# Optimization experiments

Hardware: AMD Instinct MI355X
Metric: run time of the kernel (lower is better)

The kernel has to match this reference:

```python
import jax, jax.numpy as jnp
import numpy as np

B, T, W, D, NT = 32, 512, 250, 768, 2  # batch, subtokens, words, sim_dim, num_tags


def setup_inputs() -> dict:
    key = jax.random.key(0)
    ks = jax.random.split(key, 20)
    s = 0.05
    # words_ids: 2 subtokens per word for W words, rest padding (-100)
    pos = jnp.arange(T)
    wid = jnp.where(pos < 2 * W, pos // 2, -100).astype(jnp.int64)
    words_ids = jnp.broadcast_to(wid, (B, T))
    inp = {
        'bert_out': jax.random.normal(ks[0], (B, T, D), jnp.float32),
        'words_ids': words_ids,
        'label_detect': jax.random.randint(ks[1], (B, W), 0, NT).astype(jnp.int64),
        'w_ih_l0': jax.random.normal(ks[2], (4 * D, D), jnp.float32) * s,
        'w_hh_l0': jax.random.normal(ks[3], (4 * D, D), jnp.float32) * s,
        'b_l0': jax.random.normal(ks[4], (4 * D,), jnp.float32) * s,
        'w_ih_l0r': jax.random.normal(ks[5], (4 * D, D), jnp.float32) * s,
        'w_hh_l0r': jax.random.normal(ks[6], (4 * D, D), jnp.float32) * s,
        'b_l0r': jax.random.normal(ks[7], (4 * D,), jnp.float32) * s,
        'w_ih_l1': jax.random.normal(ks[8], (4 * D, 2 * D), jnp.float32) * s,
        'w_hh_l1': jax.random.normal(ks[9], (4 * D, D), jnp.float32) * s,
        'b_l1': jax.random.normal(ks[10], (4 * D,), jnp.float32) * s,
        'w_ih_l1r': jax.random.normal(ks[11], (4 * D, 2 * D), jnp.float32) * s,
        'w_hh_l1r': jax.random.normal(ks[12], (4 * D, D), jnp.float32) * s,
        'b_l1r': jax.random.normal(ks[13], (4 * D,), jnp.float32) * s,
        'w_lin': jax.random.normal(ks[14], (NT, 2 * D), jnp.float32) * s,
        'b_lin': jax.random.normal(ks[15], (NT,), jnp.float32) * s,
        'crf_start': jax.random.normal(ks[16], (NT,), jnp.float32) * 0.1,
        'crf_end': jax.random.normal(ks[17], (NT,), jnp.float32) * 0.1,
        'crf_trans': jax.random.normal(ks[18], (NT, NT), jnp.float32) * 0.1,
    }
    return inp


def first_subtoken_gather(bert_out, words_ids):
    # For each word w in [0, W): embedding of its FIRST subtoken.
    # (matches torch.unique(sorted)+first-element-per-group on HF word_ids)
    pos = jnp.arange(T)
    mask = words_ids[:, None, :] == jnp.arange(W)[None, :, None]  # [B, W, T]
    first_idx = jnp.min(jnp.where(mask, pos[None, None, :], T - 1), axis=-1)  # [B, W]
    return jnp.take_along_axis(bert_out, first_idx[..., None], axis=1)  # [B, W, D]


def lstm_dir(x, w_ih, w_hh, b, reverse):
    # x: [B, S, In] -> [B, S, H]; PyTorch gate order i, f, g, o
    H = w_hh.shape[1]
    pre = jnp.einsum('bsi,gi->bsg', x, w_ih) + b  # b = b_ih + b_hh
    if reverse:
        pre = pre[:, ::-1]
    def step(carry, p_t):
        h, c = carry
        g = p_t + h @ w_hh.T
        i, f, gg, o = jnp.split(g, 4, axis=-1)
        c = jax.nn.sigmoid(f) * c + jax.nn.sigmoid(i) * jnp.tanh(gg)
        h = jax.nn.sigmoid(o) * jnp.tanh(c)
        return (h, c), h
    h0 = jnp.zeros((x.shape[0], H), x.dtype)
    _, hs = jax.lax.scan(step, (h0, h0), jnp.swapaxes(pre, 0, 1))
    hs = jnp.swapaxes(hs, 0, 1)
    if reverse:
        hs = hs[:, ::-1]
    return hs


def crf_log_likelihood(emis, tags, start, end, trans):
    # emis: [B, S, K]; tags: [B, S]; mask = all ones; reduction='mean'
    S = emis.shape[1]
    # numerator
    t0 = tags[:, 0]
    emis_score = jnp.sum(jnp.take_along_axis(emis, tags[..., None], axis=-1)[..., 0], axis=1)
    trans_score = jnp.sum(trans[tags[:, :-1], tags[:, 1:]], axis=1)
    num = start[t0] + emis_score + trans_score + end[tags[:, -1]]
    # partition (forward algorithm)
    alpha0 = start[None, :] + emis[:, 0]  # [B, K]
    def step(alpha, e_t):
        alpha = jax.nn.logsumexp(alpha[:, :, None] + trans[None] + e_t[:, None, :], axis=1)
        return alpha, None
    alpha, _ = jax.lax.scan(step, alpha0, jnp.swapaxes(emis[:, 1:], 0, 1))
    logZ = jax.nn.logsumexp(alpha + end[None, :], axis=-1)
    return jnp.mean(num - logZ)


def crf_decode(emis, start, end, trans):
    # Viterbi, mask = all ones. Returns [B, S] int32.
    score0 = start[None, :] + emis[:, 0]
    def fwd(score, e_t):
        cand = score[:, :, None] + trans[None]          # [B, K, K]
        bp = jnp.argmax(cand, axis=1)                    # [B, K]
        score = jnp.max(cand, axis=1) + e_t
        return score, bp
    score, hist = jax.lax.scan(fwd, score0, jnp.swapaxes(emis[:, 1:], 0, 1))
    last = jnp.argmax(score + end[None, :], axis=-1)     # [B]
    def back(tag, bp_t):
        prev = jnp.take_along_axis(bp_t, tag[:, None], axis=1)[:, 0]
        return prev, prev
    _, prevs = jax.lax.scan(back, last, hist, reverse=True)
    path = jnp.concatenate([jnp.swapaxes(prevs, 0, 1), last[:, None]], axis=1)
    return path.astype(jnp.int32)


def reference(bert_out, words_ids, label_detect,
              w_ih_l0, w_hh_l0, b_l0, w_ih_l0r, w_hh_l0r, b_l0r,
              w_ih_l1, w_hh_l1, b_l1, w_ih_l1r, w_hh_l1r, b_l1r,
              w_lin, b_lin, crf_start, crf_end, crf_trans):
    feat = first_subtoken_gather(bert_out, words_ids)                      # [B, W, D]
    h1 = jnp.concatenate([lstm_dir(feat, w_ih_l0, w_hh_l0, b_l0, False),
                          lstm_dir(feat, w_ih_l0r, w_hh_l0r, b_l0r, True)], axis=-1)
    h2 = jnp.concatenate([lstm_dir(h1, w_ih_l1, w_hh_l1, b_l1, False),
                          lstm_dir(h1, w_ih_l1r, w_hh_l1r, b_l1r, True)], axis=-1)
    logits = h2 @ w_lin.T + b_lin                                           # [B, W, 2]
    ner_prob = jax.nn.softmax(logits, axis=-1)
    llh = crf_log_likelihood(ner_prob, label_detect, crf_start, crf_end, crf_trans)
    path = crf_decode(ner_prob, crf_start, crf_end, crf_trans)
    loss = -1.0 * llh
    return path, ner_prob, loss
```

## Files before the change

### kernel.cpp

```cpp
#include <hip/hip_runtime.h>
#include <cmath>

#define B_ 32
#define T_ 512
#define W_ 250
#define D_ 768
#define H_ 768
#define G_ 3072
#define NT_ 2

__global__ void first_idx_kernel(const int* __restrict__ words_ids, int* __restrict__ fidx) {
  int i = blockIdx.x * blockDim.x + threadIdx.x;
  if (i >= B_ * W_) return;
  int b = i / W_, w = i % W_;
  const int* row = words_ids + (size_t)b * T_;
  int idx = T_ - 1;
  for (int t = 0; t < T_; ++t) {
    if (row[t] == w) { idx = t; break; }
  }
  fidx[i] = idx;
}

__global__ void gather_kernel(const float* __restrict__ bert_out, const int* __restrict__ fidx,
                              float* __restrict__ feat) {
  int i = blockIdx.x * blockDim.x + threadIdx.x;
  const int nv = D_ / 4;
  if (i >= B_ * W_ * nv) return;
  int bw = i / nv, d4 = i % nv;
  int b = bw / W_, w = bw % W_;
  int t = fidx[bw];
  float4 v = ((const float4*)(bert_out + ((size_t)b * T_ + t) * D_))[d4];
  ((float4*)(feat + ((size_t)w * B_ + b) * D_))[d4] = v;
}

__global__ __launch_bounds__(256) void gemm_bias_kernel(
    const float* __restrict__ A, const float* __restrict__ Bm,
    const float* __restrict__ bias, float* __restrict__ C,
    int M, int N, int K) {
  __shared__ float As[2][16][132];
  __shared__ float Bs[2][16][132];
  const int tid = threadIdx.x;
  const int row0 = blockIdx.x * 128;
  const int col0 = blockIdx.y * 128;
  const int tx = tid & 15;
  const int ty = tid >> 4;
  const int lr = tid >> 1;
  const int lk = (tid & 1) * 8;

  int ar = row0 + lr;
  if (ar >= M) ar = M - 1;
  const float* __restrict__ Ap = A + (size_t)ar * K + lk;
  const float* __restrict__ Bp = Bm + (size_t)(col0 + lr) * K + lk;

  float acc[8][8];
#pragma unroll
  for (int i = 0; i < 8; ++i)
#pragma unroll
    for (int j = 0; j < 8; ++j) acc[i][j] = 0.0f;

  const int nk = K >> 4;

  {
    float4 a0 = *(const float4*)(Ap + 0);
    float4 a1 = *(const float4*)(Ap + 4);
    float4 b0 = *(const float4*)(Bp + 0);
    float4 b1 = *(const float4*)(Bp + 4);
    As[0][lk + 0][lr] = a0.x; As[0][lk + 1][lr] = a0.y; As[0][lk + 2][lr] = a0.z; As[0][lk + 3][lr] = a0.w;
    As[0][lk + 4][lr] = a1.x; As[0][lk + 5][lr] = a1.y; As[0][lk + 6][lr] = a1.z; As[0][lk + 7][lr] = a1.w;
    Bs[0][lk + 0][lr] = b0.x; Bs[0][lk + 1][lr] = b0.y; Bs[0][lk + 2][lr] = b0.z; Bs[0][lk + 3][lr] = b0.w;
    Bs[0][lk + 4][lr] = b1.x; Bs[0][lk + 5][lr] = b1.y; Bs[0][lk + 6][lr] = b1.z; Bs[0][lk + 7][lr] = b1.w;
  }
  __syncthreads();

  for (int t = 0; t < nk; ++t) {
    const int cur = t & 1;
    float4 a0, a1, b0, b1;
    const bool pf = (t + 1 < nk);
    if (pf) {
      const int k0 = (t + 1) << 4;
      a0 = *(const float4*)(Ap + k0);
      a1 = *(const float4*)(Ap + k0 + 4);
      b0 = *(const float4*)(Bp + k0);
      b1 = *(const float4*)(Bp + k0 + 4);
    }
#pragma unroll
    for (int k = 0; k < 16; ++k) {
      float a[8], b[8];
      *(float4*)&a[0] = *(const float4*)&As[cur][k][ty * 8];
      *(float4*)&a[4] = *(const float4*)&As[cur][k][ty * 8 + 4];
      *(float4*)&b[0] = *(const float4*)&Bs[cur][k][tx * 8];
      *(float4*)&b[4] = *(const float4*)&Bs[cur][k][tx * 8 + 4];
#pragma unroll
      for (int i = 0; i < 8; ++i)
#pragma unroll
        for (int j = 0; j < 8; ++j) acc[i][j] += a[i] * b[j];
    }
    if (pf) {
      const int nxt = cur ^ 1;
      As[nxt][lk + 0][lr] = a0.x; As[nxt][lk + 1][lr] = a0.y; As[nxt][lk + 2][lr] = a0.z; As[nxt][lk + 3][lr] = a0.w;
      As[nxt][lk + 4][lr] = a1.x; As[nxt][lk + 5][lr] = a1.y; As[nxt][lk + 6][lr] = a1.z; As[nxt][lk + 7][lr] = a1.w;
      Bs[nxt][lk + 0][lr] = b0.x; Bs[nxt][lk + 1][lr] = b0.y; Bs[nxt][lk + 2][lr] = b0.z; Bs[nxt][lk + 3][lr] = b0.w;
      Bs[nxt][lk + 4][lr] = b1.x; Bs[nxt][lk + 5][lr] = b1.y; Bs[nxt][lk + 6][lr] = b1.z; Bs[nxt][lk + 7][lr] = b1.w;
    }
    __syncthreads();
  }

#pragma unroll
  for (int i = 0; i < 8; ++i) {
    int r = row0 + ty * 8 + i;
    if (r < M) {
#pragma unroll
      for (int j = 0; j < 8; ++j) {
        int c = col0 + tx * 8 + j;
        C[(size_t)r * N + c] = acc[i][j] + bias[c];
      }
    }
  }
}

__global__ __launch_bounds__(256) void lstm_step_kernel(
    const float* __restrict__ pre_f, const float* __restrict__ pre_r,
    const float* __restrict__ whh_f, const float* __restrict__ whh_r,
    float* __restrict__ out, float* __restrict__ hbuf, float* __restrict__ cbuf,
    int s0, int sl, int Cc) {
  const int wg = blockIdx.x;
  const int dir = wg >> 7;
  const int lw = wg & 127;
  const float* __restrict__ pre = dir ? pre_r : pre_f;
  const float* __restrict__ whh = dir ? whh_r : whh_f;
  float* hb = hbuf + (size_t)dir * 2 * B_ * H_;
  float* cb = cbuf + (size_t)dir * B_ * H_;
  const int tid = threadIdx.x;
  const int u0 = lw * 6;

  const int s = s0 + sl;
  const int w = dir ? (W_ - 1 - s) : s;
  const int prow = dir ? (Cc - 1 - sl) : sl;

  const int rgrp = tid >> 6;
  const int lane = tid & 63;
  const int kgrp = lane >> 3;
  const int bgrp = lane & 7;

  __shared__ float w_lds[24 * 860];
  __shared__ float h_lds[32 * 284];
  __shared__ float g_lds[32][24];

  const int cui = tid >> 5;
  const int cb_ = tid & 31;
  float pre_g0 = 0.f, pre_g1 = 0.f, pre_g2 = 0.f, pre_g3 = 0.f, cprev = 0.f;
  if (tid < 192) {
    const float* pbt = pre + ((size_t)prow * B_ + cb_) * G_;
    pre_g0 = pbt[0 * H_ + u0 + cui];
    pre_g1 = pbt[1 * H_ + u0 + cui];
    pre_g2 = pbt[2 * H_ + u0 + cui];
    pre_g3 = pbt[3 * H_ + u0 + cui];
    if (s > 0) cprev = cb[(size_t)cb_ * H_ + u0 + cui];
  }

  float acc[6][4];
#pragma unroll
  for (int r = 0; r < 6; ++r)
#pragma unroll
    for (int j = 0; j < 4; ++j) acc[r][j] = 0.0f;

  if (s > 0) {
#pragma unroll
    for (int v = 0; v < 18; ++v) {
      int i = v * 256 + tid;
      int r24 = i / 192;
      int f4 = i - r24 * 192;
      int k = f4 * 4;
      int grow = (r24 / 6) * H_ + u0 + (r24 % 6);
      *(float4*)&w_lds[r24 * 860 + k + 4 * (k >> 5)] =
          *(const float4*)(whh + (size_t)grow * H_ + k);
    }

    const float* __restrict__ hprev = hb + (size_t)(s & 1) * B_ * H_;
    const int kl0 = kgrp * 32;

    for (int kc = 0; kc < H_; kc += 256) {
      __syncthreads();
#pragma unroll
      for (int v = 0; v < 8; ++v) {
        int e = v * 1024 + tid * 4;
        int bb = e >> 8;
        int kk = e & 255;
        *(float4*)&h_lds[bb * 284 + kk + 4 * (kk >> 5)] =
            *(const float4*)(hprev + (size_t)bb * H_ + kc + kk);
      }
      __syncthreads();

      const int wbase = kc + kl0;
#pragma unroll 4
      for (int t = 0; t < 8; ++t) {
        const int kl = kl0 + t * 4;
        const int ka = wbase + t * 4;
        const int hoff = kl + 4 * (kl >> 5);
        const int woff = ka + 4 * (ka >> 5);
        float4 h4_0 = *(const float4*)&h_lds[(4 * bgrp + 0) * 284 + hoff];
        float4 h4_1 = *(const float4*)&h_lds[(4 * bgrp + 1) * 284 + hoff];
        float4 h4_2 = *(const float4*)&h_lds[(4 * bgrp + 2) * 284 + hoff];
        float4 h4_3 = *(const float4*)&h_lds[(4 * bgrp + 3) * 284 + hoff];
#pragma unroll
        for (int r = 0; r < 6; ++r) {
          float4 w4 = *(const float4*)&w_lds[(rgrp * 6 + r) * 860 + woff];
          acc[r][0] += h4_0.x * w4.x + h4_0.y * w4.y + h4_0.z * w4.z + h4_0.w * w4.w;
          acc[r][1] += h4_1.x * w4.x + h4_1.y * w4.y + h4_1.z * w4.z + h4_1.w * w4.w;
          acc[r][2] += h4_2.x * w4.x + h4_2.y * w4.y + h4_2.z * w4.z + h4_2.w * w4.w;
          acc[r][3] += h4_3.x * w4.x + h4_3.y * w4.y + h4_3.z * w4.z + h4_3.w * w4.w;
        }
      }
    }

#pragma unroll
    for (int r = 0; r < 6; ++r)
#pragma unroll
      for (int j = 0; j < 4; ++j) {
        float a = acc[r][j];
        a += __shfl_xor(a, 8, 64);
        a += __shfl_xor(a, 16, 64);
        a += __shfl_xor(a, 32, 64);
        acc[r][j] = a;
      }
    if (kgrp == 0) {
#pragma unroll
      for (int r = 0; r < 6; ++r)
#pragma unroll
        for (int j = 0; j < 4; ++j)
          g_lds[4 * bgrp + j][rgrp * 6 + r] = acc[r][j];
    }
  }

  __syncthreads();

  if (tid < 192) {
    float gi = pre_g0, gf = pre_g1, gg = pre_g2, go = pre_g3;
    if (s > 0) {
      gi += g_lds[cb_][cui];
      gf += g_lds[cb_][6 + cui];
      gg += g_lds[cb_][12 + cui];
      go += g_lds[cb_][18 + cui];
    }
    const float si = 1.0f / (1.0f + expf(-gi));
    const float sf = 1.0f / (1.0f + expf(-gf));
    const float so = 1.0f / (1.0f + expf(-go));
    const float c = sf * cprev + si * tanhf(gg);
    cb[(size_t)cb_ * H_ + u0 + cui] = c;
    const float h = so * tanhf(c);
    float* __restrict__ hnext = hb + (size_t)((s + 1) & 1) * B_ * H_;
    hnext[(size_t)cb_ * H_ + u0 + cui] = h;
    out[((size_t)w * B_ + cb_) * (2 * H_) + (size_t)dir * H_ + u0 + cui] = h;
  }
}

__global__ void logits_softmax_kernel(const float* __restrict__ h2, const float* __restrict__ w_lin,
                                      const float* __restrict__ b_lin, float* __restrict__ prob) {
  int i = blockIdx.x * blockDim.x + threadIdx.x;
  if (i >= B_ * W_) return;
  int b = i / W_, w = i % W_;
  const float4* x = (const float4*)(h2 + ((size_t)w * B_ + b) * (2 * H_));
  const float4* w0 = (const float4*)(w_lin);
  const float4* w1 = (const float4*)(w_lin + 2 * H_);
  float l0 = 0.f, l1 = 0.f;
#pragma unroll 4
  for (int k = 0; k < (2 * H_) / 4; ++k) {
    float4 xv = x[k];
    float4 a = w0[k];
    float4 c = w1[k];
    l0 += xv.x * a.x + xv.y * a.y + xv.z * a.z + xv.w * a.w;
    l1 += xv.x * c.x + xv.y * c.y + xv.z * c.z + xv.w * c.w;
  }
  l0 += b_lin[0];
  l1 += b_lin[1];
  float m = fmaxf(l0, l1);
  float e0 = expf(l0 - m), e1 = expf(l1 - m);
  float s = e0 + e1;
  prob[2 * (size_t)i] = e0 / s;
  prob[2 * (size_t)i + 1] = e1 / s;
}

__device__ __forceinline__ float lse2(float a, float b) {
  float m = fmaxf(a, b);
  return m + logf(expf(a - m) + expf(b - m));
}

__global__ void crf_llh_kernel(const float* __restrict__ emis, const int* __restrict__ tags,
                               const float* __restrict__ start, const float* __restrict__ endv,
                               const float* __restrict__ trans, float* __restrict__ loss_out) {
  int tid = threadIdx.x;
  float val = 0.f;
  if (tid < B_) {
    const float* e = emis + (size_t)tid * W_ * NT_;
    const int* tg = tags + (size_t)tid * W_;
    const float t00 = trans[0], t01 = trans[1], t10 = trans[2], t11 = trans[3];
    int tp = tg[0];
    float num = start[tp] + e[tp];
    float a0 = start[0] + e[0];
    float a1 = start[1] + e[1];
    for (int s = 1; s < W_; ++s) {
      int ts = tg[s];
      num += e[2 * s + ts] + trans[tp * 2 + ts];
      tp = ts;
      float n0 = lse2(a0 + t00, a1 + t10) + e[2 * s];
      float n1 = lse2(a0 + t01, a1 + t11) + e[2 * s + 1];
      a0 = n0;
      a1 = n1;
    }
    num += endv[tp];
    float logZ = lse2(a0 + endv[0], a1 + endv[1]);
    val = num - logZ;
  }
  for (int off = 32; off > 0; off >>= 1) val += __shfl_down(val, off, 64);
  if (tid == 0) loss_out[0] = -(val / (float)B_);
}

__global__ void crf_decode_kernel(const float* __restrict__ emis,
                                  const float* __restrict__ start, const float* __restrict__ endv,
                                  const float* __restrict__ trans, float* __restrict__ path_out) {
  int b = blockIdx.x * blockDim.x + threadIdx.x;
  if (b >= B_) return;
  const float* e = emis + (size_t)b * W_ * NT_;
  const float t00 = trans[0], t01 = trans[1], t10 = trans[2], t11 = trans[3];
  float s0 = start[0] + e[0];
  float s1 = start[1] + e[1];
  unsigned long long bp0[4] = {0ull, 0ull, 0ull, 0ull};
  unsigned long long bp1[4] = {0ull, 0ull, 0ull, 0ull};
  for (int s = 1; s < W_; ++s) {
    float c00 = s0 + t00, c10 = s1 + t10;
    float c01 = s0 + t01, c11 = s1 + t11;
    int b0 = (c10 > c00) ? 1 : 0;
    int b1 = (c11 > c01) ? 1 : 0;
    float m0 = b0 ? c10 : c00;
    float m1 = b1 ? c11 : c01;
    int idx = s - 1;
    bp0[idx >> 6] |= ((unsigned long long)b0) << (idx & 63);
    bp1[idx >> 6] |= ((unsigned long long)b1) << (idx & 63);
    s0 = m0 + e[2 * s];
    s1 = m1 + e[2 * s + 1];
  }
  int tag = ((s1 + endv[1]) > (s0 + endv[0])) ? 1 : 0;
  path_out[(size_t)b * W_ + (W_ - 1)] = (float)tag;
  for (int s = W_ - 2; s >= 0; --s) {
    unsigned long long word = tag ? bp1[s >> 6] : bp0[s >> 6];
    tag = (int)((word >> (s & 63)) & 1ull);
    path_out[(size_t)b * W_ + s] = (float)tag;
  }
}

extern "C" void kernel_launch(void* const* d_in, const int* in_sizes, int n_in,
                              void* d_out, int out_size, void* d_ws, size_t ws_size,
                              hipStream_t stream) {
  const float* bert_out = (const float*)d_in[0];
  const int* words_ids = (const int*)d_in[1];
  const int* label_detect = (const int*)d_in[2];
  const float* w_ih_l0 = (const float*)d_in[3];
  const float* w_hh_l0 = (const float*)d_in[4];
  const float* b_l0 = (const float*)d_in[5];
  const float* w_ih_l0r = (const float*)d_in[6];
  const float* w_hh_l0r = (const float*)d_in[7];
  const float* b_l0r = (const float*)d_in[8];
  const float* w_ih_l1 = (const float*)d_in[9];
  const float* w_hh_l1 = (const float*)d_in[10];
  const float* b_l1 = (const float*)d_in[11];
  const float* w_ih_l1r = (const float*)d_in[12];
  const float* w_hh_l1r = (const float*)d_in[13];
  const float* b_l1r = (const float*)d_in[14];
  const float* w_lin = (const float*)d_in[15];
  const float* b_lin = (const float*)d_in[16];
  const float* crf_start = (const float*)d_in[17];
  const float* crf_end = (const float*)d_in[18];
  const float* crf_trans = (const float*)d_in[19];

  float* out = (float*)d_out;
  float* path_out = out;
  float* prob_out = out + B_ * W_;
  float* loss_out = out + B_ * W_ * 3;

  auto need = [](int c) -> size_t { return 4ull * (24731456ull + 196608ull * (size_t)c); };
  int C = 10;
  if (ws_size >= need(250)) C = 250;
  else if (ws_size >= need(125)) C = 125;
  else if (ws_size >= need(50)) C = 50;
  else if (ws_size >= need(25)) C = 25;
  const int nchunk = W_ / C;
  const size_t CBG = (size_t)C * B_ * G_;

  float* h2 = (float*)d_ws;
  float* feat = h2;
  float* h1 = h2 + 12288000;
  float* preA = h1 + 12288000;
  float* preB = preA + CBG;
  float* hbuf = preB + CBG;
  float* cbuf = hbuf + 2 * 2 * B_ * H_;
  int* fidx = (int*)(cbuf + 2 * B_ * H_);

  first_idx_kernel<<<(B_ * W_ + 255) / 256, 256, 0, stream>>>(words_ids, fidx);
  gather_kernel<<<(B_ * W_ * (D_ / 4) + 255) / 256, 256, 0, stream>>>(bert_out, fidx, feat);

  const int Mc = C * B_;
  dim3 ggrid((Mc + 127) / 128, G_ / 128);

  for (int ch = 0; ch < nchunk; ++ch) {
    const int s0 = ch * C;
    gemm_bias_kernel<<<ggrid, 256, 0, stream>>>(feat + (size_t)s0 * B_ * D_, w_ih_l0, b_l0, preA, Mc, G_, D_);
    gemm_bias_kernel<<<ggrid, 256, 0, stream>>>(feat + (size_t)(W_ - C - s0) * B_ * D_, w_ih_l0r, b_l0r, preB, Mc, G_, D_);
    for (int sl = 0; sl < C; ++sl) {
      lstm_step_kernel<<<dim3(256), dim3(256), 0, stream>>>(preA, preB, w_hh_l0, w_hh_l0r, h1, hbuf, cbuf, s0, sl, C);
    }
  }

  for (int ch = 0; ch < nchunk; ++ch) {
    const int s0 = ch * C;
    gemm_bias_kernel<<<ggrid, 256, 0, stream>>>(h1 + (size_t)s0 * B_ * (2 * H_), w_ih_l1, b_l1, preA, Mc, G_, 2 * H_);
    gemm_bias_kernel<<<ggrid, 256, 0, stream>>>(h1 + (size_t)(W_ - C - s0) * B_ * (2 * H_), w_ih_l1r, b_l1r, preB, Mc, G_, 2 * H_);
    for (int sl = 0; sl < C; ++sl) {
      lstm_step_kernel<<<dim3(256), dim3(256), 0, stream>>>(preA, preB, w_hh_l1, w_hh_l1r, h2, hbuf, cbuf, s0, sl, C);
    }
  }

  logits_softmax_kernel<<<(B_ * W_ + 255) / 256, 256, 0, stream>>>(h2, w_lin, b_lin, prob_out);

  crf_llh_kernel<<<1, 64, 0, stream>>>(prob_out, label_detect, crf_start, crf_end, crf_trans, loss_out);
  crf_decode_kernel<<<1, 64, 0, stream>>>(prob_out, crf_start, crf_end, crf_trans, path_out);
}
```

Before: 11.60 ms.

## Replace per-step LSTM launches with persistent cooperative kernel using a grid counter barrier

Per-timestep launches of the LSTM recurrence are replaced by one cooperative persistent kernel per chunk. It loads the W_hh slice into LDS once, keeps the cell state in registers, and synchronises timesteps through an atomic counter barrier with agent-scope atomic loads and stores of h. This removes launch overhead and the repeated W_hh reload on every step (hundreds of launches per layer). The cost is spin-wait barrier latency and scalarised relaxed atomic loads of h. Correctness relies on relaxed atomics being visible across workgroups and on all 256 blocks being co-resident.

After: 17.39 ms. 49.9% more time.

```diff
diff --git a/kernel.cpp b/kernel.cpp
--- a/kernel.cpp
+++ b/kernel.cpp
@@ -9,8 +9,10 @@
 #define G_ 3072
 #define NT_ 2
 
-__global__ void first_idx_kernel(const int* __restrict__ words_ids, int* __restrict__ fidx) {
+__global__ void first_idx_kernel(const int* __restrict__ words_ids, int* __restrict__ fidx,
+                                 unsigned int* __restrict__ counter) {
   int i = blockIdx.x * blockDim.x + threadIdx.x;
+  if (blockIdx.x == 0 && threadIdx.x == 0) *counter = 0u;
   if (i >= B_ * W_) return;
   int b = i / W_, w = i % W_;
   const int* row = words_ids + (size_t)b * T_;
@@ -118,11 +120,11 @@
   }
 }
 
-__global__ __launch_bounds__(256) void lstm_step_kernel(
+__global__ __launch_bounds__(256) void lstm_persist_kernel(
     const float* __restrict__ pre_f, const float* __restrict__ pre_r,
     const float* __restrict__ whh_f, const float* __restrict__ whh_r,
     float* __restrict__ out, float* __restrict__ hbuf, float* __restrict__ cbuf,
-    int s0, int sl, int Cc) {
+    unsigned int* __restrict__ counter, int s0, int Cc, int ep0) {
   const int wg = blockIdx.x;
   const int dir = wg >> 7;
   const int lw = wg & 127;
@@ -133,10 +135,6 @@
   const int tid = threadIdx.x;
   const int u0 = lw * 6;
 
-  const int s = s0 + sl;
-  const int w = dir ? (W_ - 1 - s) : s;
-  const int prow = dir ? (Cc - 1 - sl) : sl;
-
   const int rgrp = tid >> 6;
   const int lane = tid & 63;
   const int kgrp = lane >> 3;
@@ -146,112 +144,137 @@
   __shared__ float h_lds[32 * 284];
   __shared__ float g_lds[32][24];
 
+#pragma unroll
+  for (int v = 0; v < 18; ++v) {
+    int i = v * 256 + tid;
+    int r24 = i / 192;
+    int f4 = i - r24 * 192;
+    int k = f4 * 4;
+    int grow = (r24 / 6) * H_ + u0 + (r24 % 6);
+    *(float4*)&w_lds[r24 * 860 + k + 4 * (k >> 5)] =
+        *(const float4*)(whh + (size_t)grow * H_ + k);
+  }
+
   const int cui = tid >> 5;
   const int cb_ = tid & 31;
-  float pre_g0 = 0.f, pre_g1 = 0.f, pre_g2 = 0.f, pre_g3 = 0.f, cprev = 0.f;
-  if (tid < 192) {
-    const float* pbt = pre + ((size_t)prow * B_ + cb_) * G_;
-    pre_g0 = pbt[0 * H_ + u0 + cui];
-    pre_g1 = pbt[1 * H_ + u0 + cui];
-    pre_g2 = pbt[2 * H_ + u0 + cui];
-    pre_g3 = pbt[3 * H_ + u0 + cui];
-    if (s > 0) cprev = cb[(size_t)cb_ * H_ + u0 + cui];
-  }
-
-  float acc[6][4];
-#pragma unroll
-  for (int r = 0; r < 6; ++r)
-#pragma unroll
-    for (int j = 0; j < 4; ++j) acc[r][j] = 0.0f;
-
-  if (s > 0) {
-#pragma unroll
-    for (int v = 0; v < 18; ++v) {
-      int i = v * 256 + tid;
-      int r24 = i / 192;
-      int f4 = i - r24 * 192;
-      int k = f4 * 4;
-      int grow = (r24 / 6) * H_ + u0 + (r24 % 6);
-      *(float4*)&w_lds[r24 * 860 + k + 4 * (k >> 5)] =
-          *(const float4*)(whh + (size_t)grow * H_ + k);
-    }
-
-    const float* __restrict__ hprev = hb + (size_t)(s & 1) * B_ * H_;
-    const int kl0 = kgrp * 32;
-
-    for (int kc = 0; kc < H_; kc += 256) {
-      __syncthreads();
-#pragma unroll
-      for (int v = 0; v < 8; ++v) {
-        int e = v * 1024 + tid * 4;
-        int bb = e >> 8;
-        int kk = e & 255;
-        *(float4*)&h_lds[bb * 284 + kk + 4 * (kk >> 5)] =
-            *(const float4*)(hprev + (size_t)bb * H_ + kc + kk);
-      }
-      __syncthreads();
-
-      const int wbase = kc + kl0;
+  float creg = 0.0f;
+  if (tid < 192 && s0 > 0) creg = cb[(size_t)cb_ * H_ + u0 + cui];
+
+  const int kl0 = kgrp * 32;
+
+  for (int sl = 0; sl < Cc; ++sl) {
+    const int s = s0 + sl;
+    const int w = dir ? (W_ - 1 - s) : s;
+    const int prow = dir ? (Cc - 1 - sl) : sl;
+
+    float pre_g0 = 0.f, pre_g1 = 0.f, pre_g2 = 0.f, pre_g3 = 0.f;
+    if (tid < 192) {
+      const float* pbt = pre + ((size_t)prow * B_ + cb_) * G_;
+      pre_g0 = pbt[0 * H_ + u0 + cui];
+      pre_g1 = pbt[1 * H_ + u0 + cui];
+      pre_g2 = pbt[2 * H_ + u0 + cui];
+      pre_g3 = pbt[3 * H_ + u0 + cui];
+    }
+
+    float acc[6][4];
+#pragma unroll
+    for (int r = 0; r < 6; ++r)
+#pragma unroll
+      for (int j = 0; j < 4; ++j) acc[r][j] = 0.0f;
+
+    if (s > 0) {
+      const float* __restrict__ hprev = hb + (size_t)(s & 1) * B_ * H_;
+      for (int kc = 0; kc < H_; kc += 256) {
+        __syncthreads();
+#pragma unroll
+        for (int v = 0; v < 8; ++v) {
+          int e = v * 1024 + tid * 4;
+          int bb = e >> 8;
+          int kk = e & 255;
+          const float* src = hprev + (size_t)bb * H_ + kc + kk;
+          float x0 = __hip_atomic_load((const float*)(src + 0), __ATOMIC_RELAXED, __HIP_MEMORY_SCOPE_AGENT);
+          float x1 = __hip_atomic_load((const float*)(src + 1), __ATOMIC_RELAXED, __HIP_MEMORY_SCOPE_AGENT);
+          float x2 = __hip_atomic_load((const float*)(src + 2), __ATOMIC_RELAXED, __HIP_MEMORY_SCOPE_AGENT);
+          float x3 = __hip_atomic_load((const float*)(src + 3), __ATOMIC_RELAXED, __HIP_MEMORY_SCOPE_AGENT);
+          int off = bb * 284 + kk + 4 * (kk >> 5);
+          h_lds[off + 0] = x0; h_lds[off + 1] = x1; h_lds[off + 2] = x2; h_lds[off + 3] = x3;
+        }
+        __syncthreads();
+
+        const int wbase = kc + kl0;
 #pragma unroll 4
-      for (int t = 0; t < 8; ++t) {
-        const int kl = kl0 + t * 4;
-        const int ka = wbase + t * 4;
-        const int hoff = kl + 4 * (kl >> 5);
-        const int woff = ka + 4 * (ka >> 5);
-        float4 h4_0 = *(const float4*)&h_lds[(4 * bgrp + 0) * 284 + hoff];
-        float4 h4_1 = *(const float4*)&h_lds[(4 * bgrp + 1) * 284 + hoff];
-        float4 h4_2 = *(const float4*)&h_lds[(4 * bgrp + 2) * 284 + hoff];
-        float4 h4_3 = *(const float4*)&h_lds[(4 * bgrp + 3) * 284 + hoff];
-#pragma unroll
-        for (int r = 0; r < 6; ++r) {
-          float4 w4 = *(const float4*)&w_lds[(rgrp * 6 + r) * 860 + woff];
-          acc[r][0] += h4_0.x * w4.x + h4_0.y * w4.y + h4_0.z * w4.z + h4_0.w * w4.w;
-          acc[r][1] += h4_1.x * w4.x + h4_1.y * w4.y + h4_1.z * w4.z + h4_1.w * w4.w;
-          acc[r][2] += h4_2.x * w4.x + h4_2.y * w4.y + h4_2.z * w4.z + h4_2.w * w4.w;
-          acc[r][3] += h4_3.x * w4.x + h4_3.y * w4.y + h4_3.z * w4.z + h4_3.w * w4.w;
+        for (int t = 0; t < 8; ++t) {
+          const int kl = kl0 + t * 4;
+          const int ka = wbase + t * 4;
+          const int hoff = kl + 4 * (kl >> 5);
+          const int woff = ka + 4 * (ka >> 5);
+          float4 h4_0 = *(const float4*)&h_lds[(4 * bgrp + 0) * 284 + hoff];
+          float4 h4_1 = *(const float4*)&h_lds[(4 * bgrp + 1) * 284 + hoff];
+          float4 h4_2 = *(const float4*)&h_lds[(4 * bgrp + 2) * 284 + hoff];
+          float4 h4_3 = *(const float4*)&h_lds[(4 * bgrp + 3) * 284 + hoff];
+#pragma unroll
+          for (int r = 0; r < 6; ++r) {
+            float4 w4 = *(const float4*)&w_lds[(rgrp * 6 + r) * 860 + woff];
+            acc[r][0] += h4_0.x * w4.x + h4_0.y * w4.y + h4_0.z * w4.z + h4_0.w * w4.w;
+            acc[r][1] += h4_1.x * w4.x + h4_1.y * w4.y + h4_1.z * w4.z + h4_1.w * w4.w;
+            acc[r][2] += h4_2.x * w4.x + h4_2.y * w4.y + h4_2.z * w4.z + h4_2.w * w4.w;
+            acc[r][3] += h4_3.x * w4.x + h4_3.y * w4.y + h4_3.z * w4.z + h4_3.w * w4.w;
+          }
         }
       }
-    }
-
-#pragma unroll
-    for (int r = 0; r < 6; ++r)
-#pragma unroll
-      for (int j = 0; j < 4; ++j) {
-        float a = acc[r][j];
-        a += __shfl_xor(a, 8, 64);
-        a += __shfl_xor(a, 16, 64);
-        a += __shfl_xor(a, 32, 64);
-        acc[r][j] = a;
+
+#pragma unroll
+      for (int r = 0; r < 6; ++r)
+#pragma unroll
+        for (int j = 0; j < 4; ++j) {
+          float a = acc[r][j];
+          a += __shfl_xor(a, 8, 64);
+          a += __shfl_xor(a, 16, 64);
+          a += __shfl_xor(a, 32, 64);
+          acc[r][j] = a;
+        }
+      if (kgrp == 0) {
+#pragma unroll
+        for (int r = 0; r < 6; ++r)
+#pragma unroll
+          for (int j = 0; j < 4; ++j)
+            g_lds[4 * bgrp + j][rgrp * 6 + r] = acc[r][j];
       }
-    if (kgrp == 0) {
-#pragma unroll
-      for (int r = 0; r < 6; ++r)
-#pragma unroll
-        for (int j = 0; j < 4; ++j)
-          g_lds[4 * bgrp + j][rgrp * 6 + r] = acc[r][j];
-    }
-  }
-
-  __syncthreads();
-
-  if (tid < 192) {
-    float gi = pre_g0, gf = pre_g1, gg = pre_g2, go = pre_g3;
-    if (s > 0) {
-      gi += g_lds[cb_][cui];
-      gf += g_lds[cb_][6 + cui];
-      gg += g_lds[cb_][12 + cui];
-      go += g_lds[cb_][18 + cui];
-    }
-    const float si = 1.0f / (1.0f + expf(-gi));
-    const float sf = 1.0f / (1.0f + expf(-gf));
-    const float so = 1.0f / (1.0f + expf(-go));
-    const float c = sf * cprev + si * tanhf(gg);
-    cb[(size_t)cb_ * H_ + u0 + cui] = c;
-    const float h = so * tanhf(c);
-    float* __restrict__ hnext = hb + (size_t)((s + 1) & 1) * B_ * H_;
-    hnext[(size_t)cb_ * H_ + u0 + cui] = h;
-    out[((size_t)w * B_ + cb_) * (2 * H_) + (size_t)dir * H_ + u0 + cui] = h;
-  }
+    }
+
+    __syncthreads();
+
+    if (tid < 192) {
+      float gi = pre_g0, gf = pre_g1, gg = pre_g2, go = pre_g3;
+      if (s > 0) {
+        gi += g_lds[cb_][cui];
+        gf += g_lds[cb_][6 + cui];
+        gg += g_lds[cb_][12 + cui];
+        go += g_lds[cb_][18 + cui];
+      }
+      const float si = 1.0f / (1.0f + expf(-gi));
+      const float sf = 1.0f / (1.0f + expf(-gf));
+      const float so = 1.0f / (1.0f + expf(-go));
+      creg = sf * creg + si * tanhf(gg);
+      const float h = so * tanhf(creg);
+      float* __restrict__ hnext = hb + (size_t)((s + 1) & 1) * B_ * H_;
+      __hip_atomic_store(&hnext[(size_t)cb_ * H_ + u0 + cui], h,
+                         __ATOMIC_RELAXED, __HIP_MEMORY_SCOPE_AGENT);
+      out[((size_t)w * B_ + cb_) * (2 * H_) + (size_t)dir * H_ + u0 + cui] = h;
+    }
+
+    __syncthreads();
+    if (tid == 0) {
+      __hip_atomic_fetch_add(counter, 1u, __ATOMIC_RELAXED, __HIP_MEMORY_SCOPE_AGENT);
+      const unsigned int tgt = 256u * (unsigned int)(ep0 + sl + 1);
+      while (__hip_atomic_load(counter, __ATOMIC_RELAXED, __HIP_MEMORY_SCOPE_AGENT) < tgt) {
+        __builtin_amdgcn_s_sleep(2);
+      }
+    }
+    __syncthreads();
+  }
+
+  if (tid < 192) cb[(size_t)cb_ * H_ + u0 + cui] = creg;
 }
 
 __global__ void logits_softmax_kernel(const float* __restrict__ h2, const float* __restrict__ w_lin,
@@ -377,7 +400,7 @@
   float* prob_out = out + B_ * W_;
   float* loss_out = out + B_ * W_ * 3;
 
-  auto need = [](int c) -> size_t { return 4ull * (24731456ull + 196608ull * (size_t)c); };
+  auto need = [](int c) -> size_t { return 4ull * (24731520ull + 196608ull * (size_t)c); };
   int C = 10;
   if (ws_size >= need(250)) C = 250;
   else if (ws_size >= need(125)) C = 125;
@@ -394,29 +417,39 @@
   float* hbuf = preB + CBG;
   float* cbuf = hbuf + 2 * 2 * B_ * H_;
   int* fidx = (int*)(cbuf + 2 * B_ * H_);
-
-  first_idx_kernel<<<(B_ * W_ + 255) / 256, 256, 0, stream>>>(words_ids, fidx);
+  unsigned int* counter = (unsigned int*)(fidx + B_ * W_);
+
+  first_idx_kernel<<<(B_ * W_ + 255) / 256, 256, 0, stream>>>(words_ids, fidx, counter);
   gather_kernel<<<(B_ * W_ * (D_ / 4) + 255) / 256, 256, 0, stream>>>(bert_out, fidx, feat);
 
   const int Mc = C * B_;
   dim3 ggrid((Mc + 127) / 128, G_ / 128);
+  int ep = 0;
 
   for (int ch = 0; ch < nchunk; ++ch) {
     const int s0 = ch * C;
     gemm_bias_kernel<<<ggrid, 256, 0, stream>>>(feat + (size_t)s0 * B_ * D_, w_ih_l0, b_l0, preA, Mc, G_, D_);
     gemm_bias_kernel<<<ggrid, 256, 0, stream>>>(feat + (size_t)(W_ - C - s0) * B_ * D_, w_ih_l0r, b_l0r, preB, Mc, G_, D_);
-    for (int sl = 0; sl < C; ++sl) {
-      lstm_step_kernel<<<dim3(256), dim3(256), 0, stream>>>(preA, preB, w_hh_l0, w_hh_l0r, h1, hbuf, cbuf, s0, sl, C);
-    }
+    const float* a0 = preA; const float* a1 = preB;
+    const float* a2 = w_hh_l0; const float* a3 = w_hh_l0r;
+    float* a4 = h1; float* a5 = hbuf; float* a6 = cbuf;
+    unsigned int* a7 = counter; int a8 = s0; int a9 = C; int a10 = ep;
+    void* args[] = {&a0, &a1, &a2, &a3, &a4, &a5, &a6, &a7, &a8, &a9, &a10};
+    hipLaunchCooperativeKernel((void*)lstm_persist_kernel, dim3(256), dim3(256), args, 0, stream);
+    ep += C;
   }
 
   for (int ch = 0; ch < nchunk; ++ch) {
     const int s0 = ch * C;
     gemm_bias_kernel<<<ggrid, 256, 0, stream>>>(h1 + (size_t)s0 * B_ * (2 * H_), w_ih_l1, b_l1, preA, Mc, G_, 2 * H_);
     gemm_bias_kernel<<<ggrid, 256, 0, stream>>>(h1 + (size_t)(W_ - C - s0) * B_ * (2 * H_), w_ih_l1r, b_l1r, preB, Mc, G_, 2 * H_);
-    for (int sl = 0; sl < C; ++sl) {
-      lstm_step_kernel<<<dim3(256), dim3(256), 0, stream>>>(preA, preB, w_hh_l1, w_hh_l1r, h2, hbuf, cbuf, s0, sl, C);
-    }
+    const float* a0 = preA; const float* a1 = preB;
+    const float* a2 = w_hh_l1; const float* a3 = w_hh_l1r;
+    float* a4 = h2; float* a5 = hbuf; float* a6 = cbuf;
+    unsigned int* a7 = counter; int a8 = s0; int a9 = C; int a10 = ep;
+    void* args[] = {&a0, &a1, &a2, &a3, &a4, &a5, &a6, &a7, &a8, &a9, &a10};
+    hipLaunchCooperativeKernel((void*)lstm_persist_kernel, dim3(256), dim3(256), args, 0, stream);
+    ep += C;
   }
 
   logits_softmax_kernel<<<(B_ * W_ + 255) / 256, 256, 0, stream>>>(h2, w_lin, b_lin, prob_out);
```
